# Kernel optimization log

Hardware: AMD Instinct MI355X
Metric: run time of the kernel (lower is better)

Reference implementation:

```python
import jax, jax.numpy as jnp
import numpy as np

N = 50000
E = 600000
IN_DIM = 256
H1, H2, H3 = 128, 64, 64
HEADS = 8


def _add_self_loops(edge_index, edge_weight=None):
    loop = jnp.arange(N, dtype=edge_index.dtype)
    src = jnp.concatenate([edge_index[0], loop])
    dst = jnp.concatenate([edge_index[1], loop])
    if edge_weight is None:
        return src, dst, None
    ew = jnp.concatenate([edge_weight, jnp.ones((N,), edge_weight.dtype)])
    return src, dst, ew


def gcn_conv(x, edge_index, edge_weight, W, b):
    # PyG GCNConv: add self-loops (weight 1), symmetric normalization, scatter-add.
    src, dst, ew = _add_self_loops(edge_index, edge_weight)
    deg = jax.ops.segment_sum(ew, dst, num_segments=N)          # [N]
    dinv = jnp.where(deg > 0, jax.lax.rsqrt(jnp.maximum(deg, 1e-12)), 0.0)
    coeff = dinv[src] * ew * dinv[dst]                          # [E+N]
    h = x @ W                                                    # [N, out]
    out = jax.ops.segment_sum(coeff[:, None] * h[src], dst, num_segments=N)
    return out + b


def gat_conv(x, edge_index, W, att_src, att_dst, b):
    # PyG GATConv, heads=HEADS, concat=False (mean over heads), leaky_relu slope 0.2.
    src, dst, _ = _add_self_loops(edge_index)
    C = W.shape[1] // HEADS
    h = (x @ W).reshape(N, HEADS, C)                             # [N,H,C]
    a_s = jnp.sum(h * att_src, axis=-1)                          # [N,H]
    a_d = jnp.sum(h * att_dst, axis=-1)                          # [N,H]
    e = jax.nn.leaky_relu(a_s[src] + a_d[dst], negative_slope=0.2)  # [E',H]
    # scatter-softmax over edges sharing a destination
    m = jax.ops.segment_max(e, dst, num_segments=N)              # [N,H]
    p = jnp.exp(e - m[dst])
    s = jax.ops.segment_sum(p, dst, num_segments=N)              # [N,H]
    alpha = p / (s[dst] + 1e-16)                                 # [E',H]
    out = jax.ops.segment_sum(alpha[:, :, None] * h[src], dst, num_segments=N)  # [N,H,C]
    return jnp.mean(out, axis=1) + b


def setup_inputs() -> dict:
    key = jax.random.key(0)
    ks = jax.random.split(key, 12)
    x = jax.random.normal(ks[0], (N, IN_DIM), dtype=jnp.float32)
    edge_index = jax.random.randint(ks[1], (2, E), 0, N, dtype=jnp.int32)
    edge_weight = jax.random.uniform(ks[2], (E,), dtype=jnp.float32)
    def glorot(k, shape):
        fan = shape[0] + shape[-1]
        return jax.random.normal(k, shape, dtype=jnp.float32) * np.sqrt(2.0 / fan)
    return {
        "x": x, "edge_index": edge_index, "edge_weight": edge_weight,
        "gc1_w": glorot(ks[3], (IN_DIM, H1)), "gc1_b": jnp.zeros((H1,), jnp.float32),
        "gat_w": glorot(ks[4], (H1, HEADS * H2)),
        "att_src": glorot(ks[5], (HEADS, H2)), "att_dst": glorot(ks[6], (HEADS, H2)),
        "gat_b": jnp.zeros((H2,), jnp.float32),
        "gc2_w": glorot(ks[7], (H2, H3)), "gc2_b": jnp.zeros((H3,), jnp.float32),
        "fc_w": glorot(ks[8], (H3, 1)), "fc_b": jnp.zeros((1,), jnp.float32),
    }


def reference(x, edge_index, edge_weight, gc1_w, gc1_b, gat_w, att_src, att_dst,
              gat_b, gc2_w, gc2_b, fc_w, fc_b):
    # dropout is inference no-op
    h = jax.nn.relu(gcn_conv(x, edge_index, edge_weight, gc1_w, gc1_b))
    h = jax.nn.relu(gat_conv(h, edge_index, gat_w, att_src, att_dst, gat_b))
    h = jax.nn.relu(gcn_conv(h, edge_index, edge_weight, gc2_w, gc2_b))
    return h @ fc_w + fc_b                                       # [N,1]
```

## Files before the change

### kernel.cpp

```cpp
#include <hip/hip_runtime.h>
#include <hip/hip_bf16.h>

#define GNN_N 50000
#define GNN_E 600000

typedef unsigned int uint;
typedef unsigned short ushort;
using short8 = __attribute__((ext_vector_type(8))) short;
using f32x4  = __attribute__((ext_vector_type(4))) float;

__device__ __forceinline__ float leaky02(float x) { return x > 0.f ? x : 0.2f * x; }
__device__ __forceinline__ ushort f2b(float f) {
    uint u = __float_as_uint(f);
    return (ushort)((u + 0x7fffu + ((u >> 16) & 1u)) >> 16);
}
__device__ __forceinline__ float b2f(ushort b) { return __uint_as_float(((uint)b) << 16); }

__global__ void gnn_hist(const int* __restrict__ dst, const float* __restrict__ ew,
                         int* __restrict__ cnt, float* __restrict__ deg, int e) {
    int i = blockIdx.x * blockDim.x + threadIdx.x;
    if (i >= e) return;
    int d = dst[i];
    atomicAdd(&cnt[d], 1);
    atomicAdd(&deg[d], ew[i]);
}
__global__ void gnn_deg_fin(float* deg, int n) {
    int i = blockIdx.x * blockDim.x + threadIdx.x;
    if (i < n) deg[i] = rsqrtf(1.0f + deg[i]);
}
__global__ void gnn_scan1(const int* __restrict__ cnt, int* __restrict__ row_ptr,
                          int* __restrict__ blksum, int n) {
    __shared__ int sh[256];
    int tid = threadIdx.x;
    int base = blockIdx.x * 1024 + tid * 4;
    int v0 = (base + 0 < n) ? cnt[base + 0] : 0;
    int v1 = (base + 1 < n) ? cnt[base + 1] : 0;
    int v2 = (base + 2 < n) ? cnt[base + 2] : 0;
    int v3 = (base + 3 < n) ? cnt[base + 3] : 0;
    int tsum = v0 + v1 + v2 + v3;
    sh[tid] = tsum;
    __syncthreads();
    for (int off = 1; off < 256; off <<= 1) {
        int t = (tid >= off) ? sh[tid - off] : 0;
        __syncthreads();
        sh[tid] += t;
        __syncthreads();
    }
    int excl = sh[tid] - tsum;
    if (base + 0 < n) row_ptr[base + 0] = excl; excl += v0;
    if (base + 1 < n) row_ptr[base + 1] = excl; excl += v1;
    if (base + 2 < n) row_ptr[base + 2] = excl; excl += v2;
    if (base + 3 < n) row_ptr[base + 3] = excl;
    if (tid == 255) blksum[blockIdx.x] = sh[255];
}
__global__ void gnn_scan2(int* blksum, int nblk, int* row_ptr_end, int total) {
    if (threadIdx.x == 0 && blockIdx.x == 0) {
        int run = 0;
        for (int b = 0; b < nblk; ++b) { int t = blksum[b]; blksum[b] = run; run += t; }
        *row_ptr_end = total;
    }
}
__global__ void gnn_scan3(int* row_ptr, const int* __restrict__ blksum, int n) {
    int i = blockIdx.x * blockDim.x + threadIdx.x;
    if (i < n) row_ptr[i] += blksum[i >> 10];
}
__global__ void gnn_scatter(const int* __restrict__ src, const int* __restrict__ dst,
                            const float* __restrict__ ew, const float* __restrict__ dinv,
                            const int* __restrict__ row_ptr, int* __restrict__ fill,
                            int* __restrict__ esrc, float* __restrict__ ecw, int e) {
    int i = blockIdx.x * blockDim.x + threadIdx.x;
    if (i >= e) return;
    int d = dst[i];
    int s = src[i];
    int pos = row_ptr[d] + atomicAdd(&fill[d], 1);
    esrc[pos] = s;
    ecw[pos] = dinv[s] * ew[i] * dinv[d];
}

__global__ void gnn_prep(const float* __restrict__ gc1_w, const float* __restrict__ gat_w,
                         const float* __restrict__ gc2_w, const float* __restrict__ att_src,
                         const float* __restrict__ att_dst, ushort* __restrict__ w1t,
                         ushort* __restrict__ w2s_t, ushort* __restrict__ w3t,
                         float* __restrict__ wa_t) {
    int t = blockIdx.x * 256 + threadIdx.x;
    if (t < 32768) {
        int k = t >> 7, n = t & 127;
        w1t[n * 256 + k] = f2b(gc1_w[t]);
        return;
    }
    t -= 32768;
    if (t < 65536) {
        int c = t >> 10, r = t & 1023;
        int h = r >> 7, k = r & 127;
        w2s_t[t] = f2b(0.125f * gat_w[(size_t)k * 512 + h * 64 + c]);
        return;
    }
    t -= 65536;
    if (t < 4096) {
        int k = t >> 6, n = t & 63;
        w3t[n * 64 + k] = f2b(gc2_w[t]);
        return;
    }
    t -= 4096;
    if (t < 2048) {
        int j = t >> 7, k = t & 127;
        int h = j & 7;
        const float* av = (j < 8) ? att_src : att_dst;
        float s = 0.f;
        for (int c = 0; c < 64; ++c) s += gat_w[(size_t)k * 512 + h * 64 + c] * av[h * 64 + c];
        wa_t[j * 128 + k] = s;
    }
}

template <bool AF32, bool BIAS>
__global__ __launch_bounds__(256) void gnn_mfma_gemm(const void* __restrict__ Av,
                                                     const ushort* __restrict__ Bt,
                                                     ushort* __restrict__ C,
                                                     const float* __restrict__ bias,
                                                     int M, int N, int K) {
    __shared__ ushort As[64 * 40];
    __shared__ ushort Bs[64 * 40];
    const int tid = threadIdx.x;
    const int wv = tid >> 6, lane = tid & 63;
    const int g = lane >> 4, r = lane & 15;
    const int brow = blockIdx.y << 6, bcol = blockIdx.x << 6;

    const int srow = tid >> 2;
    const int skoff = (tid & 3) << 3;
    int arow = brow + srow;
    if (arow >= M) arow = M - 1;
    const ushort* A16 = (const ushort*)Av;
    const float*  A32 = (const float*)Av;
    const ushort* Ap16 = A16 + (size_t)arow * K + skoff;
    const float*  Ap32 = A32 + (size_t)arow * K + skoff;
    const ushort* Bp = Bt + (size_t)(bcol + srow) * K + skoff;
    ushort* AsW = &As[srow * 40 + skoff];
    ushort* BsW = &Bs[srow * 40 + skoff];

    f32x4 acc[4] = {};

    for (int k0 = 0; k0 < K; k0 += 32) {
        if constexpr (AF32) {
            float4 f0 = *(const float4*)(Ap32 + k0);
            float4 f1 = *(const float4*)(Ap32 + k0 + 4);
            short8 t;
            t[0] = (short)f2b(f0.x); t[1] = (short)f2b(f0.y);
            t[2] = (short)f2b(f0.z); t[3] = (short)f2b(f0.w);
            t[4] = (short)f2b(f1.x); t[5] = (short)f2b(f1.y);
            t[6] = (short)f2b(f1.z); t[7] = (short)f2b(f1.w);
            *(short8*)AsW = t;
        } else {
            *(short8*)AsW = *(const short8*)(Ap16 + k0);
        }
        *(short8*)BsW = *(const short8*)(Bp + k0);
        __syncthreads();
        short8 bfrag = *(const short8*)&Bs[(wv * 16 + r) * 40 + g * 8];
#pragma unroll
        for (int mb = 0; mb < 4; ++mb) {
            short8 afrag = *(const short8*)&As[(mb * 16 + r) * 40 + g * 8];
            acc[mb] = __builtin_amdgcn_mfma_f32_16x16x32_bf16(afrag, bfrag, acc[mb], 0, 0, 0);
        }
        __syncthreads();
    }

    const int col = bcol + wv * 16 + r;
    float bv = 0.f;
    if constexpr (BIAS) bv = bias[col];
#pragma unroll
    for (int mb = 0; mb < 4; ++mb) {
        int rowb = brow + mb * 16 + g * 4;
#pragma unroll
        for (int rr = 0; rr < 4; ++rr) {
            int row = rowb + rr;
            if (row < M) {
                float val = acc[mb][rr];
                if constexpr (BIAS) {
                    val += bv;
                    val = val > 0.f ? val : 0.f;
                }
                C[(size_t)row * N + col] = f2b(val);
            }
        }
    }
}

__global__ __launch_bounds__(256) void gnn_gcn_node128_asd(const int* __restrict__ row_ptr,
                                                           const int* __restrict__ esrc,
                                                           const float* __restrict__ ecw,
                                                           const float* __restrict__ dinv,
                                                           const ushort* __restrict__ hb,
                                                           const float* __restrict__ b,
                                                           const float* __restrict__ wa,
                                                           ushort* __restrict__ out,
                                                           float* __restrict__ a_s,
                                                           float* __restrict__ a_d, int n) {
    __shared__ float swa[16 * 128];
    for (int i = threadIdx.x; i < 16 * 128; i += 256) swa[i] = wa[i];
    __syncthreads();
    int v = blockIdx.x * 4 + (threadIdx.x >> 6);
    int lane = threadIdx.x & 63;
    if (v >= n) return;
    float di = dinv[v];
    float sc = di * di;
    uint us = *(const uint*)(hb + (size_t)v * 128 + 2 * lane);
    float acc0 = sc * __uint_as_float(us << 16);
    float acc1 = sc * __uint_as_float(us & 0xffff0000u);
    int beg = row_ptr[v], end = row_ptr[v + 1];
    int p = beg;
    for (; p + 8 <= end; p += 8) {
        int s[8]; float c[8]; uint u[8];
#pragma unroll
        for (int t = 0; t < 8; ++t) s[t] = esrc[p + t];
#pragma unroll
        for (int t = 0; t < 8; ++t) c[t] = ecw[p + t];
#pragma unroll
        for (int t = 0; t < 8; ++t) u[t] = *(const uint*)(hb + (size_t)s[t] * 128 + 2 * lane);
#pragma unroll
        for (int t = 0; t < 8; ++t) {
            acc0 += c[t] * __uint_as_float(u[t] << 16);
            acc1 += c[t] * __uint_as_float(u[t] & 0xffff0000u);
        }
    }
    for (; p < end; ++p) {
        int s = esrc[p];
        float cw = ecw[p];
        uint u = *(const uint*)(hb + (size_t)s * 128 + 2 * lane);
        acc0 += cw * __uint_as_float(u << 16);
        acc1 += cw * __uint_as_float(u & 0xffff0000u);
    }
    float o0 = acc0 + b[2 * lane];
    float o1 = acc1 + b[2 * lane + 1];
    o0 = o0 > 0.f ? o0 : 0.f;
    o1 = o1 > 0.f ? o1 : 0.f;
    uint o = (uint)f2b(o0) | ((uint)f2b(o1) << 16);
    *(uint*)(out + (size_t)v * 128 + 2 * lane) = o;

    float part[16];
#pragma unroll
    for (int j = 0; j < 16; ++j)
        part[j] = o0 * swa[j * 128 + 2 * lane] + o1 * swa[j * 128 + 2 * lane + 1];
#pragma unroll
    for (int m = 1; m < 64; m <<= 1) {
#pragma unroll
        for (int j = 0; j < 16; ++j) part[j] += __shfl_xor(part[j], m);
    }
    if (lane == 0) {
#pragma unroll
        for (int j = 0; j < 8; ++j) {
            a_s[(size_t)v * 8 + j] = part[j];
            a_d[(size_t)v * 8 + j] = part[8 + j];
        }
    }
}

__global__ __launch_bounds__(256) void gnn_gat_z(const int* __restrict__ row_ptr,
                                                 const int* __restrict__ esrc,
                                                 const float* __restrict__ a_s,
                                                 const float* __restrict__ a_d,
                                                 const ushort* __restrict__ g1b,
                                                 ushort* __restrict__ zb, int n) {
    int v = blockIdx.x * 4 + (threadIdx.x >> 6);
    int lane = threadIdx.x & 63;
    if (v >= n) return;
    const int hh = lane & 7;
    const float adh = a_d[(size_t)v * 8 + hh];

    float z0[8] = {}, z1[8] = {};
    float sl;
    {
        float pv = __expf(leaky02(a_s[(size_t)v * 8 + hh] + adh));
        uint u = *(const uint*)(g1b + (size_t)v * 128 + 2 * lane);
        float g0 = __uint_as_float(u << 16);
        float g1v = __uint_as_float(u & 0xffff0000u);
        sl = pv;
        float ph[8];
#pragma unroll
        for (int h = 0; h < 8; ++h) ph[h] = __shfl(pv, h);
#pragma unroll
        for (int h = 0; h < 8; ++h) { z0[h] += ph[h] * g0; z1[h] += ph[h] * g1v; }
    }
    int beg = row_ptr[v], end = row_ptr[v + 1];
    int p = beg;
    for (; p + 4 <= end; p += 4) {
        int s[4]; float e[4]; uint u[4];
#pragma unroll
        for (int t = 0; t < 4; ++t) s[t] = esrc[p + t];
#pragma unroll
        for (int t = 0; t < 4; ++t) e[t] = a_s[(size_t)s[t] * 8 + hh];
#pragma unroll
        for (int t = 0; t < 4; ++t) u[t] = *(const uint*)(g1b + (size_t)s[t] * 128 + 2 * lane);
#pragma unroll
        for (int t = 0; t < 4; ++t) {
            float pv = __expf(leaky02(e[t] + adh));
            sl += pv;
            float g0 = __uint_as_float(u[t] << 16);
            float g1v = __uint_as_float(u[t] & 0xffff0000u);
            float ph[8];
#pragma unroll
            for (int h = 0; h < 8; ++h) ph[h] = __shfl(pv, h);
#pragma unroll
            for (int h = 0; h < 8; ++h) { z0[h] += ph[h] * g0; z1[h] += ph[h] * g1v; }
        }
    }
    for (; p < end; ++p) {
        int s = esrc[p];
        float pv = __expf(leaky02(a_s[(size_t)s * 8 + hh] + adh));
        uint u = *(const uint*)(g1b + (size_t)s * 128 + 2 * lane);
        sl += pv;
        float g0 = __uint_as_float(u << 16);
        float g1v = __uint_as_float(u & 0xffff0000u);
        float ph[8];
#pragma unroll
        for (int h = 0; h < 8; ++h) ph[h] = __shfl(pv, h);
#pragma unroll
        for (int h = 0; h < 8; ++h) { z0[h] += ph[h] * g0; z1[h] += ph[h] * g1v; }
    }
    float slx = sl + 1e-16f;
#pragma unroll
    for (int h = 0; h < 8; ++h) {
        float rs = 1.f / __shfl(slx, h);
        uint o = (uint)f2b(z0[h] * rs) | ((uint)f2b(z1[h] * rs) << 16);
        *(uint*)(zb + (size_t)v * 1024 + h * 128 + 2 * lane) = o;
    }
}

__global__ __launch_bounds__(256) void gnn_gcn_node64_fc(const int* __restrict__ row_ptr,
                                                         const int* __restrict__ esrc,
                                                         const float* __restrict__ ecw,
                                                         const float* __restrict__ dinv,
                                                         const ushort* __restrict__ hb,
                                                         const float* __restrict__ b,
                                                         const float* __restrict__ fc_w,
                                                         const float* __restrict__ fc_b,
                                                         float* __restrict__ out, int n) {
    int v = blockIdx.x * 4 + (threadIdx.x >> 6);
    int lane = threadIdx.x & 63;
    if (v >= n) return;
    float di = dinv[v];
    float acc = di * di * b2f(hb[(size_t)v * 64 + lane]);
    int beg = row_ptr[v], end = row_ptr[v + 1];
    int p = beg;
    for (; p + 8 <= end; p += 8) {
        int s[8]; float c[8]; ushort hv[8];
#pragma unroll
        for (int t = 0; t < 8; ++t) s[t] = esrc[p + t];
#pragma unroll
        for (int t = 0; t < 8; ++t) c[t] = ecw[p + t];
#pragma unroll
        for (int t = 0; t < 8; ++t) hv[t] = hb[(size_t)s[t] * 64 + lane];
#pragma unroll
        for (int t = 0; t < 8; ++t) acc += c[t] * b2f(hv[t]);
    }
    for (; p < end; ++p) {
        int s = esrc[p];
        acc += ecw[p] * b2f(hb[(size_t)s * 64 + lane]);
    }
    float o = acc + b[lane];
    o = o > 0.f ? o : 0.f;
    float val = o * fc_w[lane];
#pragma unroll
    for (int m = 32; m; m >>= 1) val += __shfl_xor(val, m);
    if (lane == 0) out[v] = val + fc_b[0];
}

extern "C" void kernel_launch(void* const* d_in, const int* in_sizes, int n_in,
                              void* d_out, int out_size, void* d_ws, size_t ws_size,
                              hipStream_t stream) {
    const float* x       = (const float*)d_in[0];
    const int*   ei      = (const int*)d_in[1];
    const float* ew      = (const float*)d_in[2];
    const float* gc1_w   = (const float*)d_in[3];
    const float* gc1_b   = (const float*)d_in[4];
    const float* gat_w   = (const float*)d_in[5];
    const float* att_src = (const float*)d_in[6];
    const float* att_dst = (const float*)d_in[7];
    const float* gat_b   = (const float*)d_in[8];
    const float* gc2_w   = (const float*)d_in[9];
    const float* gc2_b   = (const float*)d_in[10];
    const float* fc_w    = (const float*)d_in[11];
    const float* fc_b    = (const float*)d_in[12];
    float* out = (float*)d_out;

    const int N = GNN_N;
    const int E = in_sizes[2];
    const int* src = ei;
    const int* dst = ei + E;

    char* p = (char*)d_ws;
    ushort* zb  = (ushort*)p; p += (size_t)N * 1024 * 2;
    ushort* h1b = (ushort*)p; p += (size_t)N * 128 * 2;
    ushort* g1b = (ushort*)p; p += (size_t)N * 128 * 2;
    ushort* g2b = (ushort*)p; p += (size_t)N * 64 * 2;
    ushort* h3b = (ushort*)p; p += (size_t)N * 64 * 2;
    ushort* w1t = (ushort*)p; p += (size_t)128 * 256 * 2;
    ushort* w2s_t = (ushort*)p; p += (size_t)64 * 1024 * 2;
    ushort* w3t = (ushort*)p; p += (size_t)64 * 64 * 2;
    float*  wa_t = (float*)p; p += 16 * 128 * 4;
    float*  a_s = (float*)p;  p += (size_t)N * 8 * 4;
    float*  a_d = (float*)p;  p += (size_t)N * 8 * 4;
    int* row_ptr = (int*)p;   p += (size_t)(N + 64) * 4;
    int* esrc = (int*)p;      p += (size_t)E * 4;
    float* ecw = (float*)p;   p += (size_t)E * 4;
    int* cnt = (int*)p;       p += (size_t)N * 4;
    int* fill = (int*)p;      p += (size_t)N * 4;
    float* dinv = (float*)p;  p += (size_t)N * 4;
    int* blksum = (int*)p;    p += 4096;

    auto cdiv = [](long a, long b) { return (int)((a + b - 1) / b); };

    hipMemsetAsync(cnt, 0, (size_t)N * 12, stream);
    gnn_hist<<<cdiv(E, 256), 256, 0, stream>>>(dst, ew, cnt, dinv, E);
    gnn_deg_fin<<<cdiv(N, 256), 256, 0, stream>>>(dinv, N);
    const int nblk = cdiv(N, 1024);
    gnn_scan1<<<nblk, 256, 0, stream>>>(cnt, row_ptr, blksum, N);
    gnn_scan2<<<1, 64, 0, stream>>>(blksum, nblk, row_ptr + N, E);
    gnn_scan3<<<cdiv(N, 256), 256, 0, stream>>>(row_ptr, blksum, N);
    gnn_scatter<<<cdiv(E, 256), 256, 0, stream>>>(src, dst, ew, dinv, row_ptr, fill, esrc, ecw, E);

    gnn_prep<<<408, 256, 0, stream>>>(gc1_w, gat_w, gc2_w, att_src, att_dst, w1t, w2s_t, w3t, wa_t);

    {
        dim3 grid(128 / 64, cdiv(N, 64));
        gnn_mfma_gemm<true, false><<<grid, 256, 0, stream>>>(x, w1t, h1b, nullptr, N, 128, 256);
    }
    gnn_gcn_node128_asd<<<cdiv(N, 4), 256, 0, stream>>>(row_ptr, esrc, ecw, dinv, h1b, gc1_b,
                                                        wa_t, g1b, a_s, a_d, N);

    gnn_gat_z<<<cdiv(N, 4), 256, 0, stream>>>(row_ptr, esrc, a_s, a_d, g1b, zb, N);
    {
        dim3 grid(1, cdiv(N, 64));
        gnn_mfma_gemm<false, true><<<grid, 256, 0, stream>>>(zb, w2s_t, g2b, gat_b, N, 64, 1024);
    }

    {
        dim3 grid(1, cdiv(N, 64));
        gnn_mfma_gemm<false, false><<<grid, 256, 0, stream>>>(g2b, w3t, h3b, nullptr, N, 64, 64);
    }
    gnn_gcn_node64_fc<<<cdiv(N, 4), 256, 0, stream>>>(row_ptr, esrc, ecw, dinv, h3b, gc2_b,
                                                      fc_w, fc_b, out, N);
}
```

Baseline: 348.1 us.

## Split wavefront into two half-waves processing alternate edges in gather kernels

Each 64-lane wavefront in the three per-node gather kernels (GCN layer 1, GAT aggregation, GCN layer 2 + FC) is split into two 32-lane halves. Each half handles alternating edges and loads wider vectors (uint2 or uint) per lane, and the halves combine their partial sums with a cross-half shuffle at the end. The aim is to double the edges in flight per wavefront and use wider memory transactions for the latency-bound neighbour gathers. In exchange it adds extra shuffle reductions, doubles the per-lane accumulator registers in the GAT kernel (32 floats), and leaves idle lanes at the store.

```diff
diff --git a/kernel.cpp b/kernel.cpp
--- a/kernel.cpp
+++ b/kernel.cpp
@@ -15,6 +15,8 @@
     return (ushort)((u + 0x7fffu + ((u >> 16) & 1u)) >> 16);
 }
 __device__ __forceinline__ float b2f(ushort b) { return __uint_as_float(((uint)b) << 16); }
+__device__ __forceinline__ float blo(uint u) { return __uint_as_float(u << 16); }
+__device__ __forceinline__ float bhi(uint u) { return __uint_as_float(u & 0xffff0000u); }
 
 __global__ void gnn_hist(const int* __restrict__ dst, const float* __restrict__ ew,
                          int* __restrict__ cnt, float* __restrict__ deg, int e) {
@@ -200,47 +202,70 @@
     int v = blockIdx.x * 4 + (threadIdx.x >> 6);
     int lane = threadIdx.x & 63;
     if (v >= n) return;
+    const int sl = lane & 31;
+    const int half = lane >> 5;
     float di = dinv[v];
-    float sc = di * di;
-    uint us = *(const uint*)(hb + (size_t)v * 128 + 2 * lane);
-    float acc0 = sc * __uint_as_float(us << 16);
-    float acc1 = sc * __uint_as_float(us & 0xffff0000u);
+    float a0, a1, a2, a3;
+    {
+        float scl = half ? 0.f : di * di;
+        uint2 u = *(const uint2*)(hb + (size_t)v * 128 + 4 * sl);
+        a0 = scl * blo(u.x); a1 = scl * bhi(u.x);
+        a2 = scl * blo(u.y); a3 = scl * bhi(u.y);
+    }
     int beg = row_ptr[v], end = row_ptr[v + 1];
-    int p = beg;
-    for (; p + 8 <= end; p += 8) {
-        int s[8]; float c[8]; uint u[8];
-#pragma unroll
-        for (int t = 0; t < 8; ++t) s[t] = esrc[p + t];
-#pragma unroll
-        for (int t = 0; t < 8; ++t) c[t] = ecw[p + t];
-#pragma unroll
-        for (int t = 0; t < 8; ++t) u[t] = *(const uint*)(hb + (size_t)s[t] * 128 + 2 * lane);
-#pragma unroll
-        for (int t = 0; t < 8; ++t) {
-            acc0 += c[t] * __uint_as_float(u[t] << 16);
-            acc1 += c[t] * __uint_as_float(u[t] & 0xffff0000u);
-        }
-    }
-    for (; p < end; ++p) {
-        int s = esrc[p];
-        float cw = ecw[p];
-        uint u = *(const uint*)(hb + (size_t)s * 128 + 2 * lane);
-        acc0 += cw * __uint_as_float(u << 16);
-        acc1 += cw * __uint_as_float(u & 0xffff0000u);
-    }
-    float o0 = acc0 + b[2 * lane];
-    float o1 = acc1 + b[2 * lane + 1];
-    o0 = o0 > 0.f ? o0 : 0.f;
-    o1 = o1 > 0.f ? o1 : 0.f;
-    uint o = (uint)f2b(o0) | ((uint)f2b(o1) << 16);
-    *(uint*)(out + (size_t)v * 128 + 2 * lane) = o;
+    int cntE = end - beg;
+    int pairs = cntE >> 1;
+    int i = 0;
+    for (; i + 4 <= pairs; i += 4) {
+        int s[4]; float c[4]; uint2 u[4];
+#pragma unroll
+        for (int t = 0; t < 4; ++t) s[t] = esrc[beg + 2 * (i + t) + half];
+#pragma unroll
+        for (int t = 0; t < 4; ++t) c[t] = ecw[beg + 2 * (i + t) + half];
+#pragma unroll
+        for (int t = 0; t < 4; ++t) u[t] = *(const uint2*)(hb + (size_t)s[t] * 128 + 4 * sl);
+#pragma unroll
+        for (int t = 0; t < 4; ++t) {
+            a0 += c[t] * blo(u[t].x); a1 += c[t] * bhi(u[t].x);
+            a2 += c[t] * blo(u[t].y); a3 += c[t] * bhi(u[t].y);
+        }
+    }
+    for (; i < pairs; ++i) {
+        int s = esrc[beg + 2 * i + half];
+        float c = ecw[beg + 2 * i + half];
+        uint2 u = *(const uint2*)(hb + (size_t)s * 128 + 4 * sl);
+        a0 += c * blo(u.x); a1 += c * bhi(u.x);
+        a2 += c * blo(u.y); a3 += c * bhi(u.y);
+    }
+    if (cntE & 1) {
+        int s = esrc[end - 1];
+        float c = half ? 0.f : ecw[end - 1];
+        uint2 u = *(const uint2*)(hb + (size_t)s * 128 + 4 * sl);
+        a0 += c * blo(u.x); a1 += c * bhi(u.x);
+        a2 += c * blo(u.y); a3 += c * bhi(u.y);
+    }
+    a0 += __shfl_xor(a0, 32); a1 += __shfl_xor(a1, 32);
+    a2 += __shfl_xor(a2, 32); a3 += __shfl_xor(a3, 32);
+
+    float4 bv = *(const float4*)(b + 4 * sl);
+    float o0 = a0 + bv.x, o1 = a1 + bv.y, o2 = a2 + bv.z, o3 = a3 + bv.w;
+    o0 = o0 > 0.f ? o0 : 0.f; o1 = o1 > 0.f ? o1 : 0.f;
+    o2 = o2 > 0.f ? o2 : 0.f; o3 = o3 > 0.f ? o3 : 0.f;
+    if (lane < 32) {
+        uint2 w;
+        w.x = (uint)f2b(o0) | ((uint)f2b(o1) << 16);
+        w.y = (uint)f2b(o2) | ((uint)f2b(o3) << 16);
+        *(uint2*)(out + (size_t)v * 128 + 4 * sl) = w;
+    }
 
     float part[16];
 #pragma unroll
-    for (int j = 0; j < 16; ++j)
-        part[j] = o0 * swa[j * 128 + 2 * lane] + o1 * swa[j * 128 + 2 * lane + 1];
-#pragma unroll
-    for (int m = 1; m < 64; m <<= 1) {
+    for (int j = 0; j < 16; ++j) {
+        const float* wj = &swa[j * 128 + 4 * sl];
+        part[j] = o0 * wj[0] + o1 * wj[1] + o2 * wj[2] + o3 * wj[3];
+    }
+#pragma unroll
+    for (int m = 1; m < 32; m <<= 1) {
 #pragma unroll
         for (int j = 0; j < 16; ++j) part[j] += __shfl_xor(part[j], m);
     }
@@ -262,65 +287,102 @@
     int v = blockIdx.x * 4 + (threadIdx.x >> 6);
     int lane = threadIdx.x & 63;
     if (v >= n) return;
+    const int sl = lane & 31;
+    const int half = lane >> 5;
     const int hh = lane & 7;
+    const int hbase = lane & 32;
     const float adh = a_d[(size_t)v * 8 + hh];
 
-    float z0[8] = {}, z1[8] = {};
-    float sl;
+    float z0[8] = {}, z1[8] = {}, z2[8] = {}, z3[8] = {};
+    float sloc = 0.f;
     {
         float pv = __expf(leaky02(a_s[(size_t)v * 8 + hh] + adh));
-        uint u = *(const uint*)(g1b + (size_t)v * 128 + 2 * lane);
-        float g0 = __uint_as_float(u << 16);
-        float g1v = __uint_as_float(u & 0xffff0000u);
-        sl = pv;
+        if (half) pv = 0.f;
+        sloc += pv;
+        uint2 u = *(const uint2*)(g1b + (size_t)v * 128 + 4 * sl);
+        float g0 = blo(u.x), g1v = bhi(u.x), g2v = blo(u.y), g3v = bhi(u.y);
         float ph[8];
 #pragma unroll
-        for (int h = 0; h < 8; ++h) ph[h] = __shfl(pv, h);
-#pragma unroll
-        for (int h = 0; h < 8; ++h) { z0[h] += ph[h] * g0; z1[h] += ph[h] * g1v; }
+        for (int h = 0; h < 8; ++h) ph[h] = __shfl(pv, hbase | h);
+#pragma unroll
+        for (int h = 0; h < 8; ++h) {
+            z0[h] += ph[h] * g0; z1[h] += ph[h] * g1v;
+            z2[h] += ph[h] * g2v; z3[h] += ph[h] * g3v;
+        }
     }
     int beg = row_ptr[v], end = row_ptr[v + 1];
-    int p = beg;
-    for (; p + 4 <= end; p += 4) {
-        int s[4]; float e[4]; uint u[4];
-#pragma unroll
-        for (int t = 0; t < 4; ++t) s[t] = esrc[p + t];
-#pragma unroll
-        for (int t = 0; t < 4; ++t) e[t] = a_s[(size_t)s[t] * 8 + hh];
-#pragma unroll
-        for (int t = 0; t < 4; ++t) u[t] = *(const uint*)(g1b + (size_t)s[t] * 128 + 2 * lane);
-#pragma unroll
-        for (int t = 0; t < 4; ++t) {
+    int cntE = end - beg;
+    int pairs = cntE >> 1;
+    int i = 0;
+    for (; i + 2 <= pairs; i += 2) {
+        int s[2]; float e[2]; uint2 u[2];
+#pragma unroll
+        for (int t = 0; t < 2; ++t) s[t] = esrc[beg + 2 * (i + t) + half];
+#pragma unroll
+        for (int t = 0; t < 2; ++t) e[t] = a_s[(size_t)s[t] * 8 + hh];
+#pragma unroll
+        for (int t = 0; t < 2; ++t) u[t] = *(const uint2*)(g1b + (size_t)s[t] * 128 + 4 * sl);
+#pragma unroll
+        for (int t = 0; t < 2; ++t) {
             float pv = __expf(leaky02(e[t] + adh));
-            sl += pv;
-            float g0 = __uint_as_float(u[t] << 16);
-            float g1v = __uint_as_float(u[t] & 0xffff0000u);
+            sloc += pv;
+            float g0 = blo(u[t].x), g1v = bhi(u[t].x), g2v = blo(u[t].y), g3v = bhi(u[t].y);
             float ph[8];
 #pragma unroll
-            for (int h = 0; h < 8; ++h) ph[h] = __shfl(pv, h);
-#pragma unroll
-            for (int h = 0; h < 8; ++h) { z0[h] += ph[h] * g0; z1[h] += ph[h] * g1v; }
-        }
-    }
-    for (; p < end; ++p) {
-        int s = esrc[p];
+            for (int h = 0; h < 8; ++h) ph[h] = __shfl(pv, hbase | h);
+#pragma unroll
+            for (int h = 0; h < 8; ++h) {
+                z0[h] += ph[h] * g0; z1[h] += ph[h] * g1v;
+                z2[h] += ph[h] * g2v; z3[h] += ph[h] * g3v;
+            }
+        }
+    }
+    for (; i < pairs; ++i) {
+        int s = esrc[beg + 2 * i + half];
         float pv = __expf(leaky02(a_s[(size_t)s * 8 + hh] + adh));
-        uint u = *(const uint*)(g1b + (size_t)s * 128 + 2 * lane);
-        sl += pv;
-        float g0 = __uint_as_float(u << 16);
-        float g1v = __uint_as_float(u & 0xffff0000u);
+        sloc += pv;
+        uint2 u = *(const uint2*)(g1b + (size_t)s * 128 + 4 * sl);
+        float g0 = blo(u.x), g1v = bhi(u.x), g2v = blo(u.y), g3v = bhi(u.y);
         float ph[8];
 #pragma unroll
-        for (int h = 0; h < 8; ++h) ph[h] = __shfl(pv, h);
-#pragma unroll
-        for (int h = 0; h < 8; ++h) { z0[h] += ph[h] * g0; z1[h] += ph[h] * g1v; }
-    }
-    float slx = sl + 1e-16f;
+        for (int h = 0; h < 8; ++h) ph[h] = __shfl(pv, hbase | h);
+#pragma unroll
+        for (int h = 0; h < 8; ++h) {
+            z0[h] += ph[h] * g0; z1[h] += ph[h] * g1v;
+            z2[h] += ph[h] * g2v; z3[h] += ph[h] * g3v;
+        }
+    }
+    if (cntE & 1) {
+        int s = esrc[end - 1];
+        float pv = __expf(leaky02(a_s[(size_t)s * 8 + hh] + adh));
+        if (half) pv = 0.f;
+        sloc += pv;
+        uint2 u = *(const uint2*)(g1b + (size_t)s * 128 + 4 * sl);
+        float g0 = blo(u.x), g1v = bhi(u.x), g2v = blo(u.y), g3v = bhi(u.y);
+        float ph[8];
+#pragma unroll
+        for (int h = 0; h < 8; ++h) ph[h] = __shfl(pv, hbase | h);
+#pragma unroll
+        for (int h = 0; h < 8; ++h) {
+            z0[h] += ph[h] * g0; z1[h] += ph[h] * g1v;
+            z2[h] += ph[h] * g2v; z3[h] += ph[h] * g3v;
+        }
+    }
+    float slx = sloc + __shfl_xor(sloc, 32) + 1e-16f;
 #pragma unroll
     for (int h = 0; h < 8; ++h) {
-        float rs = 1.f / __shfl(slx, h);
-        uint o = (uint)f2b(z0[h] * rs) | ((uint)f2b(z1[h] * rs) << 16);
-        *(uint*)(zb + (size_t)v * 1024 + h * 128 + 2 * lane) = o;
+        z0[h] += __shfl_xor(z0[h], 32); z1[h] += __shfl_xor(z1[h], 32);
+        z2[h] += __shfl_xor(z2[h], 32); z3[h] += __shfl_xor(z3[h], 32);
+    }
+    if (lane < 32) {
+#pragma unroll
+        for (int h = 0; h < 8; ++h) {
+            float rs = 1.f / __shfl(slx, h);
+            uint2 w;
+            w.x = (uint)f2b(z0[h] * rs) | ((uint)f2b(z1[h] * rs) << 16);
+            w.y = (uint)f2b(z2[h] * rs) | ((uint)f2b(z3[h] * rs) << 16);
+            *(uint2*)(zb + (size_t)v * 1024 + h * 128 + 4 * sl) = w;
+        }
     }
 }
 
@@ -336,30 +398,51 @@
     int v = blockIdx.x * 4 + (threadIdx.x >> 6);
     int lane = threadIdx.x & 63;
     if (v >= n) return;
+    const int sl = lane & 31;
+    const int half = lane >> 5;
     float di = dinv[v];
-    float acc = di * di * b2f(hb[(size_t)v * 64 + lane]);
+    float a0, a1;
+    {
+        float scl = half ? 0.f : di * di;
+        uint u = *(const uint*)(hb + (size_t)v * 64 + 2 * sl);
+        a0 = scl * blo(u); a1 = scl * bhi(u);
+    }
     int beg = row_ptr[v], end = row_ptr[v + 1];
-    int p = beg;
-    for (; p + 8 <= end; p += 8) {
-        int s[8]; float c[8]; ushort hv[8];
-#pragma unroll
-        for (int t = 0; t < 8; ++t) s[t] = esrc[p + t];
-#pragma unroll
-        for (int t = 0; t < 8; ++t) c[t] = ecw[p + t];
-#pragma unroll
-        for (int t = 0; t < 8; ++t) hv[t] = hb[(size_t)s[t] * 64 + lane];
-#pragma unroll
-        for (int t = 0; t < 8; ++t) acc += c[t] * b2f(hv[t]);
-    }
-    for (; p < end; ++p) {
-        int s = esrc[p];
-        acc += ecw[p] * b2f(hb[(size_t)s * 64 + lane]);
-    }
-    float o = acc + b[lane];
-    o = o > 0.f ? o : 0.f;
-    float val = o * fc_w[lane];
-#pragma unroll
-    for (int m = 32; m; m >>= 1) val += __shfl_xor(val, m);
+    int cntE = end - beg;
+    int pairs = cntE >> 1;
+    int i = 0;
+    for (; i + 4 <= pairs; i += 4) {
+        int s[4]; float c[4]; uint u[4];
+#pragma unroll
+        for (int t = 0; t < 4; ++t) s[t] = esrc[beg + 2 * (i + t) + half];
+#pragma unroll
+        for (int t = 0; t < 4; ++t) c[t] = ecw[beg + 2 * (i + t) + half];
+#pragma unroll
+        for (int t = 0; t < 4; ++t) u[t] = *(const uint*)(hb + (size_t)s[t] * 64 + 2 * sl);
+#pragma unroll
+        for (int t = 0; t < 4; ++t) { a0 += c[t] * blo(u[t]); a1 += c[t] * bhi(u[t]); }
+    }
+    for (; i < pairs; ++i) {
+        int s = esrc[beg + 2 * i + half];
+        float c = ecw[beg + 2 * i + half];
+        uint u = *(const uint*)(hb + (size_t)s * 64 + 2 * sl);
+        a0 += c * blo(u); a1 += c * bhi(u);
+    }
+    if (cntE & 1) {
+        int s = esrc[end - 1];
+        float c = half ? 0.f : ecw[end - 1];
+        uint u = *(const uint*)(hb + (size_t)s * 64 + 2 * sl);
+        a0 += c * blo(u); a1 += c * bhi(u);
+    }
+    a0 += __shfl_xor(a0, 32);
+    a1 += __shfl_xor(a1, 32);
+    float o0 = a0 + b[2 * sl];
+    float o1 = a1 + b[2 * sl + 1];
+    o0 = o0 > 0.f ? o0 : 0.f;
+    o1 = o1 > 0.f ? o1 : 0.f;
+    float val = o0 * fc_w[2 * sl] + o1 * fc_w[2 * sl + 1];
+#pragma unroll
+    for (int m = 1; m < 32; m <<= 1) val += __shfl_xor(val, m);
     if (lane == 0) out[v] = val + fc_b[0];
 }
 
```

New measurement: 338.3 us. 2.8% less time.
